# Kernel tuning notes

Measured on AMD Instinct MI355X. Metric: run time of the kernel, lower is better.

Reference implementation:

```python
import jax, jax.numpy as jnp
import numpy as np

CLIP = 1.3   # FastSign STE clamp range (FracBNN-style)
EPS = 1e-5   # BatchNorm eps

@jax.custom_vjp
def fast_sign(x):
    # forward: sign(x); backward: straight-through grad of clamp(x, -1.3, 1.3)
    return jnp.sign(x)

def _fs_fwd(x):
    return jnp.sign(x), x

def _fs_bwd(res, g):
    return (g * (jnp.abs(res) <= CLIP).astype(g.dtype),)

fast_sign.defvjp(_fs_fwd, _fs_bwd)

def conv(x, w, pad):
    return jax.lax.conv_general_dilated(
        x, w, window_strides=(1, 1), padding=[(pad, pad), (pad, pad)],
        dimension_numbers=('NCHW', 'OIHW', 'NCHW'))

def bn(x, gamma, beta, mean, var):
    # eval-mode BatchNorm2d folded into a single scale/shift
    inv = gamma * jax.lax.rsqrt(var + EPS)
    return x * inv[None, :, None, None] + (beta - mean * inv)[None, :, None, None]

def setup_inputs() -> dict:
    key = jax.random.key(0)
    ks = jax.random.split(key, 11)
    C = 32
    x = jax.random.normal(ks[0], (32, C, 160, 160), jnp.float32)
    w3 = jax.random.normal(ks[1], (C, C, 3, 3), jnp.float32) * 0.1
    g3 = jax.random.uniform(ks[2], (C,), jnp.float32, 0.5, 1.5)
    b3 = jax.random.normal(ks[3], (C,), jnp.float32) * 0.1
    m3 = jax.random.normal(ks[4], (C,), jnp.float32) * 0.1
    v3 = jax.random.uniform(ks[5], (C,), jnp.float32, 0.5, 1.5)
    w1 = jax.random.normal(ks[6], (C, C, 1, 1), jnp.float32) * 0.1
    g1 = jax.random.uniform(ks[7], (C,), jnp.float32, 0.5, 1.5)
    b1 = jax.random.normal(ks[8], (C,), jnp.float32) * 0.1
    m1 = jax.random.normal(ks[9], (C,), jnp.float32) * 0.1
    v1 = jax.random.uniform(ks[10], (C,), jnp.float32, 0.5, 1.5)
    return {"x": x, "w3": w3, "g3": g3, "b3": b3, "m3": m3, "v3": v3,
            "w1": w1, "g1": g1, "b1": b1, "m1": m1, "v1": v1}

def reference(x, w3, g3, b3, m3, v3, w1, g1, b1, m1, v1):
    # block 1: binarize -> 3x3 binary conv -> BN -> residual
    y = bn(conv(fast_sign(x), fast_sign(w3), 1), g3, b3, m3, v3) + x
    # block 2: binarize -> 1x1 binary conv -> BN -> residual
    z = bn(conv(fast_sign(y), fast_sign(w1), 0), g1, b1, m1, v1) + y
    return z
```

## Files before the change

### kernel.cpp

```cpp
#include <hip/hip_runtime.h>
#include <stdint.h>

#define C   32
#define H   160
#define W   160
#define NB  32
#define HW  (H * W)
#define CHW (C * HW)
#define NPIX (NB * HW)


__global__ void pack_params(const float* __restrict__ w3,
                            const float* __restrict__ g3, const float* __restrict__ b3,
                            const float* __restrict__ m3, const float* __restrict__ v3,
                            const float* __restrict__ w1,
                            const float* __restrict__ g1, const float* __restrict__ b1,
                            const float* __restrict__ m1, const float* __restrict__ v1,
                            uint32_t* __restrict__ wsu) {
    int t = threadIdx.x;
    if (t < 288) {
        int oc = t / 9, tap = t % 9;
        uint32_t bits = 0;
#pragma unroll
        for (int ic = 0; ic < 32; ++ic)
            bits |= (w3[oc * 288 + ic * 9 + tap] < 0.0f) ? (1u << ic) : 0u;
        wsu[t] = bits;
    } else if (t < 320) {
        int oc = t - 288;
        uint32_t bits = 0;
#pragma unroll
        for (int ic = 0; ic < 32; ++ic)
            bits |= (w1[oc * 32 + ic] < 0.0f) ? (1u << ic) : 0u;
        wsu[288 + oc] = bits;
        float* f = (float*)wsu;
        float inv3 = g3[oc] * rsqrtf(v3[oc] + 1e-5f);
        f[320 + oc] = inv3;
        f[352 + oc] = b3[oc] - m3[oc] * inv3;
        float inv1 = g1[oc] * rsqrtf(v1[oc] + 1e-5f);
        f[384 + oc] = inv1;
        f[416 + oc] = b1[oc] - m1[oc] * inv1;
    }
}

__global__ __launch_bounds__(256) void pack_x(const float* __restrict__ x,
                                              uint32_t* __restrict__ xbits) {
    int i = blockIdx.x * blockDim.x + threadIdx.x;
    if (i >= NPIX / 4) return;
    int p = i * 4;
    int n = p / HW;
    int r = p % HW;
    const float* xp = x + n * CHW + r;
    uint32_t b0 = 0, b1 = 0, b2 = 0, b3 = 0;
#pragma unroll
    for (int c = 0; c < 32; ++c) {
        float4 v = *reinterpret_cast<const float4*>(xp + c * HW);
        b0 |= (v.x < 0.0f) ? (1u << c) : 0u;
        b1 |= (v.y < 0.0f) ? (1u << c) : 0u;
        b2 |= (v.z < 0.0f) ? (1u << c) : 0u;
        b3 |= (v.w < 0.0f) ? (1u << c) : 0u;
    }
    *reinterpret_cast<uint4*>(xbits + p) = make_uint4(b0, b1, b2, b3);
}

__global__ __launch_bounds__(256) void fused_block(const float* __restrict__ x,
                                                   const uint32_t* __restrict__ wsu,
                                                   float* __restrict__ out) {
    __shared__ uint32_t swb3[288];
    __shared__ uint32_t swb1[32];
    __shared__ float    sp[128];

    {
        int t = threadIdx.x;
        if (t < 256) swb3[t] = wsu[t];
        if (t < 32) { swb3[256 + t] = wsu[256 + t]; swb1[t] = wsu[288 + t]; }
        if (t < 128) sp[t] = ((const float*)wsu)[320 + t];
    }
    __syncthreads();

    int pi = blockIdx.x * blockDim.x + threadIdx.x;
    if (pi >= NPIX / 2) return;
    int p0  = pi * 2;
    int n   = p0 / HW;
    int rem = p0 % HW;
    int h   = rem / W;
    int w   = rem % W;

    const uint32_t* xbn = wsu + 448 + n * HW;

    uint32_t nb[3][4];
    const bool r0ok = (h > 0), r2ok = (h < H - 1);
    const bool c0ok = (w > 0), c3ok = (w < W - 2);
#pragma unroll
    for (int r = 0; r < 3; ++r) {
        bool rok = (r == 0) ? r0ok : (r == 2) ? r2ok : true;
        const uint32_t* rp = xbn + (h + r - 1) * W + w;
        if (rok) {
            nb[r][0] = c0ok ? rp[-1] : 0u;
            nb[r][1] = rp[0];
            nb[r][2] = rp[1];
            nb[r][3] = c3ok ? rp[2] : 0u;
        } else {
            nb[r][0] = 0u; nb[r][1] = 0u; nb[r][2] = 0u; nb[r][3] = 0u;
        }
    }

    const float* xrow = x + n * CHW + h * W + w;
    float y0[32], y1[32];

    if (r0ok && r2ok && c0ok && c3ok) {
#pragma unroll
        for (int oc = 0; oc < 32; ++oc) {
            int s0 = 0, s1 = 0;
#pragma unroll
            for (int r = 0; r < 3; ++r) {
#pragma unroll
                for (int c = 0; c < 3; ++c) {
                    uint32_t wv = swb3[oc * 9 + r * 3 + c];
                    s0 += __popc(nb[r][c] ^ wv);
                    s1 += __popc(nb[r][c + 1] ^ wv);
                }
            }
            float sc = sp[oc], sh = sp[32 + oc];
            float2 xv = *reinterpret_cast<const float2*>(xrow + oc * HW);
            y0[oc] = fmaf((float)(288 - 2 * s0), sc, sh) + xv.x;
            y1[oc] = fmaf((float)(288 - 2 * s1), sc, sh) + xv.y;
        }
    } else {
        int cm0 = c0ok ? -1 : 0, cm3 = c3ok ? -1 : 0;
        int m[3][4];
#pragma unroll
        for (int r = 0; r < 3; ++r) {
            bool rok = (r == 0) ? r0ok : (r == 2) ? r2ok : true;
            int rm = rok ? -1 : 0;
            m[r][0] = rm & cm0; m[r][1] = rm; m[r][2] = rm; m[r][3] = rm & cm3;
        }
#pragma unroll
        for (int oc = 0; oc < 32; ++oc) {
            int s0 = 0, s1 = 0;
#pragma unroll
            for (int r = 0; r < 3; ++r) {
#pragma unroll
                for (int c = 0; c < 3; ++c) {
                    uint32_t wv = swb3[oc * 9 + r * 3 + c];
                    s0 += (32 - 2 * __popc(nb[r][c] ^ wv)) & m[r][c];
                    s1 += (32 - 2 * __popc(nb[r][c + 1] ^ wv)) & m[r][c + 1];
                }
            }
            float sc = sp[oc], sh = sp[32 + oc];
            float2 xv = *reinterpret_cast<const float2*>(xrow + oc * HW);
            y0[oc] = fmaf((float)s0, sc, sh) + xv.x;
            y1[oc] = fmaf((float)s1, sc, sh) + xv.y;
        }
    }

    uint32_t yb0 = 0, yb1 = 0;
#pragma unroll
    for (int oc = 0; oc < 32; ++oc) {
        yb0 |= (y0[oc] < 0.0f) ? (1u << oc) : 0u;
        yb1 |= (y1[oc] < 0.0f) ? (1u << oc) : 0u;
    }
    float* orow = out + n * CHW + h * W + w;
#pragma unroll
    for (int oc = 0; oc < 32; ++oc) {
        float sc = sp[64 + oc], sh = sp[96 + oc];
        int c0 = 32 - 2 * __popc(yb0 ^ swb1[oc]);
        int c1 = 32 - 2 * __popc(yb1 ^ swb1[oc]);
        float2 zv;
        zv.x = fmaf((float)c0, sc, sh) + y0[oc];
        zv.y = fmaf((float)c1, sc, sh) + y1[oc];
        *reinterpret_cast<float2*>(orow + oc * HW) = zv;
    }
}

extern "C" void kernel_launch(void* const* d_in, const int* in_sizes, int n_in,
                              void* d_out, int out_size, void* d_ws, size_t ws_size,
                              hipStream_t stream) {
    const float* x  = (const float*)d_in[0];
    const float* w3 = (const float*)d_in[1];
    const float* g3 = (const float*)d_in[2];
    const float* b3 = (const float*)d_in[3];
    const float* m3 = (const float*)d_in[4];
    const float* v3 = (const float*)d_in[5];
    const float* w1 = (const float*)d_in[6];
    const float* g1 = (const float*)d_in[7];
    const float* b1 = (const float*)d_in[8];
    const float* m1 = (const float*)d_in[9];
    const float* v1 = (const float*)d_in[10];
    float* out = (float*)d_out;
    uint32_t* wsu = (uint32_t*)d_ws;

    pack_params<<<1, 320, 0, stream>>>(w3, g3, b3, m3, v3, w1, g1, b1, m1, v1, wsu);
    pack_x<<<NPIX / 4 / 256, 256, 0, stream>>>(x, wsu + 448);
    fused_block<<<NPIX / 2 / 256, 256, 0, stream>>>(x, wsu, out);
}
```

Baseline: 104.0 us.

## Split border pixels into separate fix-up kernel and read weights via scalar loads

```diff
diff --git a/kernel.cpp b/kernel.cpp
--- a/kernel.cpp
+++ b/kernel.cpp
@@ -8,6 +8,7 @@
 #define HW  (H * W)
 #define CHW (C * HW)
 #define NPIX (NB * HW)
+#define XBOFF 448
 
 
 __global__ void pack_params(const float* __restrict__ w3,
@@ -62,95 +63,53 @@
     *reinterpret_cast<uint4*>(xbits + p) = make_uint4(b0, b1, b2, b3);
 }
 
-__global__ __launch_bounds__(256) void fused_block(const float* __restrict__ x,
-                                                   const uint32_t* __restrict__ wsu,
-                                                   float* __restrict__ out) {
-    __shared__ uint32_t swb3[288];
-    __shared__ uint32_t swb1[32];
-    __shared__ float    sp[128];
-
-    {
-        int t = threadIdx.x;
-        if (t < 256) swb3[t] = wsu[t];
-        if (t < 32) { swb3[256 + t] = wsu[256 + t]; swb1[t] = wsu[288 + t]; }
-        if (t < 128) sp[t] = ((const float*)wsu)[320 + t];
-    }
-    __syncthreads();
-
+__global__ __launch_bounds__(256) void fused_main(const float* __restrict__ x,
+                                                  const uint32_t* __restrict__ wsu,
+                                                  float* __restrict__ out) {
+    const float* wf = (const float*)wsu;
     int pi = blockIdx.x * blockDim.x + threadIdx.x;
-    if (pi >= NPIX / 2) return;
     int p0  = pi * 2;
     int n   = p0 / HW;
     int rem = p0 % HW;
     int h   = rem / W;
     int w   = rem % W;
 
-    const uint32_t* xbn = wsu + 448 + n * HW;
+    const uint32_t* xbn = wsu + XBOFF + n * HW;
+
+    int hm1 = (h > 0) ? h - 1 : 0;
+    int hp1 = (h < H - 1) ? h + 1 : H - 1;
+    int wm1 = (w > 0) ? w - 1 : 0;
+    int wp2 = (w < W - 2) ? w + 2 : W - 1;
 
     uint32_t nb[3][4];
-    const bool r0ok = (h > 0), r2ok = (h < H - 1);
-    const bool c0ok = (w > 0), c3ok = (w < W - 2);
-#pragma unroll
-    for (int r = 0; r < 3; ++r) {
-        bool rok = (r == 0) ? r0ok : (r == 2) ? r2ok : true;
-        const uint32_t* rp = xbn + (h + r - 1) * W + w;
-        if (rok) {
-            nb[r][0] = c0ok ? rp[-1] : 0u;
-            nb[r][1] = rp[0];
-            nb[r][2] = rp[1];
-            nb[r][3] = c3ok ? rp[2] : 0u;
-        } else {
-            nb[r][0] = 0u; nb[r][1] = 0u; nb[r][2] = 0u; nb[r][3] = 0u;
-        }
+    {
+        const uint32_t* r0 = xbn + hm1 * W;
+        const uint32_t* r1 = xbn + h   * W;
+        const uint32_t* r2 = xbn + hp1 * W;
+        nb[0][0] = r0[wm1]; nb[0][1] = r0[w]; nb[0][2] = r0[w + 1]; nb[0][3] = r0[wp2];
+        nb[1][0] = r1[wm1]; nb[1][1] = r1[w]; nb[1][2] = r1[w + 1]; nb[1][3] = r1[wp2];
+        nb[2][0] = r2[wm1]; nb[2][1] = r2[w]; nb[2][2] = r2[w + 1]; nb[2][3] = r2[wp2];
     }
 
     const float* xrow = x + n * CHW + h * W + w;
     float y0[32], y1[32];
 
-    if (r0ok && r2ok && c0ok && c3ok) {
-#pragma unroll
-        for (int oc = 0; oc < 32; ++oc) {
-            int s0 = 0, s1 = 0;
-#pragma unroll
-            for (int r = 0; r < 3; ++r) {
-#pragma unroll
-                for (int c = 0; c < 3; ++c) {
-                    uint32_t wv = swb3[oc * 9 + r * 3 + c];
-                    s0 += __popc(nb[r][c] ^ wv);
-                    s1 += __popc(nb[r][c + 1] ^ wv);
-                }
+#pragma unroll
+    for (int oc = 0; oc < 32; ++oc) {
+        int s0 = 0, s1 = 0;
+#pragma unroll
+        for (int r = 0; r < 3; ++r) {
+#pragma unroll
+            for (int c = 0; c < 3; ++c) {
+                uint32_t wv = wsu[oc * 9 + r * 3 + c];
+                s0 += __popc(nb[r][c] ^ wv);
+                s1 += __popc(nb[r][c + 1] ^ wv);
             }
-            float sc = sp[oc], sh = sp[32 + oc];
-            float2 xv = *reinterpret_cast<const float2*>(xrow + oc * HW);
-            y0[oc] = fmaf((float)(288 - 2 * s0), sc, sh) + xv.x;
-            y1[oc] = fmaf((float)(288 - 2 * s1), sc, sh) + xv.y;
         }
-    } else {
-        int cm0 = c0ok ? -1 : 0, cm3 = c3ok ? -1 : 0;
-        int m[3][4];
-#pragma unroll
-        for (int r = 0; r < 3; ++r) {
-            bool rok = (r == 0) ? r0ok : (r == 2) ? r2ok : true;
-            int rm = rok ? -1 : 0;
-            m[r][0] = rm & cm0; m[r][1] = rm; m[r][2] = rm; m[r][3] = rm & cm3;
-        }
-#pragma unroll
-        for (int oc = 0; oc < 32; ++oc) {
-            int s0 = 0, s1 = 0;
-#pragma unroll
-            for (int r = 0; r < 3; ++r) {
-#pragma unroll
-                for (int c = 0; c < 3; ++c) {
-                    uint32_t wv = swb3[oc * 9 + r * 3 + c];
-                    s0 += (32 - 2 * __popc(nb[r][c] ^ wv)) & m[r][c];
-                    s1 += (32 - 2 * __popc(nb[r][c + 1] ^ wv)) & m[r][c + 1];
-                }
-            }
-            float sc = sp[oc], sh = sp[32 + oc];
-            float2 xv = *reinterpret_cast<const float2*>(xrow + oc * HW);
-            y0[oc] = fmaf((float)s0, sc, sh) + xv.x;
-            y1[oc] = fmaf((float)s1, sc, sh) + xv.y;
-        }
+        float sc = wf[320 + oc], sh = wf[352 + oc];
+        float2 xv = *reinterpret_cast<const float2*>(xrow + oc * HW);
+        y0[oc] = fmaf((float)(288 - 2 * s0), sc, sh) + xv.x;
+        y1[oc] = fmaf((float)(288 - 2 * s1), sc, sh) + xv.y;
     }
 
     uint32_t yb0 = 0, yb1 = 0;
@@ -162,13 +121,69 @@
     float* orow = out + n * CHW + h * W + w;
 #pragma unroll
     for (int oc = 0; oc < 32; ++oc) {
-        float sc = sp[64 + oc], sh = sp[96 + oc];
-        int c0 = 32 - 2 * __popc(yb0 ^ swb1[oc]);
-        int c1 = 32 - 2 * __popc(yb1 ^ swb1[oc]);
+        float sc = wf[384 + oc], sh = wf[416 + oc];
+        int c0 = 32 - 2 * __popc(yb0 ^ wsu[288 + oc]);
+        int c1 = 32 - 2 * __popc(yb1 ^ wsu[288 + oc]);
         float2 zv;
         zv.x = fmaf((float)c0, sc, sh) + y0[oc];
         zv.y = fmaf((float)c1, sc, sh) + y1[oc];
         *reinterpret_cast<float2*>(orow + oc * HW) = zv;
+    }
+}
+
+__global__ __launch_bounds__(256) void border_fix(const float* __restrict__ x,
+                                                  const uint32_t* __restrict__ wsu,
+                                                  float* __restrict__ out) {
+    const float* wf = (const float*)wsu;
+    int t = blockIdx.x * blockDim.x + threadIdx.x;
+    if (t >= NB * 636) return;
+    int n = t / 636, idx = t % 636;
+    int h, w;
+    if (idx < 160)      { h = 0;         w = idx; }
+    else if (idx < 320) { h = H - 1;     w = idx - 160; }
+    else if (idx < 478) { h = idx - 319; w = 0; }
+    else                { h = idx - 477; w = W - 1; }
+
+    const uint32_t* xbn = wsu + XBOFF + n * HW;
+    uint32_t nb[3][3];
+    int m[3][3];
+#pragma unroll
+    for (int r = 0; r < 3; ++r) {
+        int hh = h + r - 1;
+        bool rok = (hh >= 0) && (hh < H);
+#pragma unroll
+        for (int c = 0; c < 3; ++c) {
+            int ww = w + c - 1;
+            bool ok = rok && (ww >= 0) && (ww < W);
+            m[r][c]  = ok ? -1 : 0;
+            nb[r][c] = ok ? xbn[hh * W + ww] : 0u;
+        }
+    }
+
+    const float* xp = x + n * CHW + h * W + w;
+    float y[32];
+    uint32_t yb = 0;
+#pragma unroll
+    for (int oc = 0; oc < 32; ++oc) {
+        int s = 0;
+#pragma unroll
+        for (int r = 0; r < 3; ++r) {
+#pragma unroll
+            for (int c = 0; c < 3; ++c) {
+                uint32_t wv = wsu[oc * 9 + r * 3 + c];
+                s += (32 - 2 * __popc(nb[r][c] ^ wv)) & m[r][c];
+            }
+        }
+        float sc = wf[320 + oc], sh = wf[352 + oc];
+        y[oc] = fmaf((float)s, sc, sh) + xp[oc * HW];
+        yb |= (y[oc] < 0.0f) ? (1u << oc) : 0u;
+    }
+    float* op = out + n * CHW + h * W + w;
+#pragma unroll
+    for (int oc = 0; oc < 32; ++oc) {
+        float sc = wf[384 + oc], sh = wf[416 + oc];
+        int cc = 32 - 2 * __popc(yb ^ wsu[288 + oc]);
+        op[oc * HW] = fmaf((float)cc, sc, sh) + y[oc];
     }
 }
 
@@ -190,6 +205,7 @@
     uint32_t* wsu = (uint32_t*)d_ws;
 
     pack_params<<<1, 320, 0, stream>>>(w3, g3, b3, m3, v3, w1, g1, b1, m1, v1, wsu);
-    pack_x<<<NPIX / 4 / 256, 256, 0, stream>>>(x, wsu + 448);
-    fused_block<<<NPIX / 2 / 256, 256, 0, stream>>>(x, wsu, out);
-}
+    pack_x<<<NPIX / 4 / 256, 256, 0, stream>>>(x, wsu + XBOFF);
+    fused_main<<<NPIX / 2 / 256, 256, 0, stream>>>(x, wsu, out);
+    border_fix<<<(NB * 636 + 255) / 256, 256, 0, stream>>>(x, wsu, out);
+}
```

New measurement: 84.43 us. -18.8%, faster.
